# Optimization experiments

Measured on AMD Instinct MI355X. Metric: run time of the kernel, lower is better.

## Reference

```python
import jax, jax.numpy as jnp
import numpy as np

H = 128; TIME_DIM = 8; LAM = 0.01; NUM_LAYERS = 2; B = 64
N_FACT = 100000; N_COMP = 5000; E = 500000; D_FACT = 384; D_COMP = 64
MLP_IN = 2 + 2 * (TIME_DIM // 2) + 1  # 11


def setup_inputs() -> dict:
    key = jax.random.key(0)
    ks = jax.random.split(key, 40)
    rn = lambda k, sh, s=0.05: jax.random.normal(k, sh, jnp.float32) * s
    inp = {
        'x_fact': jax.random.normal(ks[0], (N_FACT, D_FACT), jnp.float32),
        'x_comp': jax.random.normal(ks[1], (N_COMP, D_COMP), jnp.float32),
        'ea_f2c': jax.random.uniform(ks[2], (E, 2), jnp.float32),
        'ea_c2f': jax.random.uniform(ks[3], (E, 2), jnp.float32),
        'ei_f2c_src': jax.random.randint(ks[4], (E,), 0, N_FACT, jnp.int32),
        'ei_f2c_dst': jax.random.randint(ks[5], (E,), 0, N_COMP, jnp.int32),
        'ei_c2f_src': jax.random.randint(ks[6], (E,), 0, N_COMP, jnp.int32),
        'ei_c2f_dst': jax.random.randint(ks[7], (E,), 0, N_FACT, jnp.int32),
        'fact_batch': jnp.sort(jax.random.randint(ks[8], (N_FACT,), 0, B, jnp.int32)),
        'comp_batch': jnp.sort(jax.random.randint(ks[9], (N_COMP,), 0, B, jnp.int32)),
        # lazy per-type input projections
        'W_in_fact': rn(ks[10], (D_FACT, H)), 'b_in_fact': jnp.zeros((H,), jnp.float32),
        'W_in_comp': rn(ks[11], (D_COMP, H)), 'b_in_comp': jnp.zeros((H,), jnp.float32),
        # EdgeAttrEncoder MLP: 11 -> 32 -> 16 -> 1
        'eW1': rn(ks[12], (MLP_IN, 32)), 'eb1': jnp.zeros((32,), jnp.float32),
        'eW2': rn(ks[13], (32, 16)), 'eb2': jnp.zeros((16,), jnp.float32),
        'eW3': rn(ks[14], (16, 1)), 'eb3': jnp.zeros((1,), jnp.float32),
        # GraphConv per layer (axis0) per edge type (axis1: 0=f->c, 1=c->f)
        'W_rel': rn(ks[15], (NUM_LAYERS, 2, H, H)), 'b_rel': jnp.zeros((NUM_LAYERS, 2, H), jnp.float32),
        'W_root': rn(ks[16], (NUM_LAYERS, 2, H, H)),
        # shared post LayerNorm per node type (axis0: 0=fact, 1=company)
        'ln_scale': jnp.ones((2, H), jnp.float32), 'ln_bias': jnp.zeros((2, H), jnp.float32),
        # classifier 2H -> H -> 1
        'Wc1': rn(ks[17], (2 * H, H)), 'bc1': jnp.zeros((H,), jnp.float32),
        'Wc2': rn(ks[18], (H, 1)), 'bc2': jnp.zeros((1,), jnp.float32),
    }
    return inp


def _edge_gate(ea, eW1, eb1, eW2, eb2, eW3, eb3):
    # ea: [E,2] -> gate [E]
    sent = jnp.clip(ea[:, 0:1], -1.0, 1.0)
    decay = ea[:, 1:2]
    # decay in [0,1] -> delta_t = -log(decay)/lambda, clamped >= 0
    dt = jnp.maximum(-jnp.log(jnp.clip(decay, 1e-6, None)) / LAM, 0.0)
    ds = jnp.clip(dt / 30.0, 0.0, 12.0)
    freqs = jnp.arange(1, TIME_DIM // 2 + 1, dtype=ds.dtype)
    tvec = jnp.concatenate([jnp.sin(ds * freqs), jnp.cos(ds * freqs), ds], axis=-1)
    x = jnp.concatenate([sent, jnp.log1p(dt), tvec], axis=-1)  # [E,11]
    h = jax.nn.relu(x @ eW1 + eb1)
    h = jax.nn.relu(h @ eW2 + eb2)
    return jax.nn.sigmoid(h @ eW3 + eb3)[:, 0]


def _layernorm(x, scale, bias, eps=1e-5):
    mu = jnp.mean(x, axis=-1, keepdims=True)
    var = jnp.var(x, axis=-1, keepdims=True)
    return (x - mu) * jax.lax.rsqrt(var + eps) * scale + bias


def _seg_mean(x, seg, n):
    s = jax.ops.segment_sum(x, seg, num_segments=n)
    c = jax.ops.segment_sum(jnp.ones((x.shape[0], 1), x.dtype), seg, num_segments=n)
    return s / jnp.maximum(c, 1.0)


def reference(x_fact, x_comp, ea_f2c, ea_c2f, ei_f2c_src, ei_f2c_dst, ei_c2f_src,
              ei_c2f_dst, fact_batch, comp_batch, W_in_fact, b_in_fact, W_in_comp,
              b_in_comp, eW1, eb1, eW2, eb2, eW3, eb3, W_rel, b_rel, W_root,
              ln_scale, ln_bias, Wc1, bc1, Wc2, bc2):
    # per-type input projection + ReLU
    xf = jax.nn.relu(x_fact @ W_in_fact + b_in_fact)   # [N_fact, H]
    xc = jax.nn.relu(x_comp @ W_in_comp + b_in_comp)   # [N_comp, H]
    # MLP-gated edge weights (shared encoder across relations)
    w_f2c = _edge_gate(ea_f2c, eW1, eb1, eW2, eb2, eW3, eb3)  # [E]
    w_c2f = _edge_gate(ea_c2f, eW1, eb1, eW2, eb2, eW3, eb3)  # [E]
    nf, nc = xf.shape[0], xc.shape[0]
    for l in range(NUM_LAYERS):
        prev_f, prev_c = xf, xc
        # GraphConv: lin_rel(sum_j w_ij * x_j) + lin_root(x_i)  (aggr='add')
        agg_c = jax.ops.segment_sum(xf[ei_f2c_src] * w_f2c[:, None], ei_f2c_dst, num_segments=nc)
        new_c = agg_c @ W_rel[l, 0] + b_rel[l, 0] + xc @ W_root[l, 0]
        agg_f = jax.ops.segment_sum(xc[ei_c2f_src] * w_c2f[:, None], ei_c2f_dst, num_segments=nf)
        new_f = agg_f @ W_rel[l, 1] + b_rel[l, 1] + xf @ W_root[l, 1]
        # ReLU -> residual -> shared per-type LayerNorm
        xf = _layernorm(jax.nn.relu(new_f) + prev_f, ln_scale[0], ln_bias[0])
        xc = _layernorm(jax.nn.relu(new_c) + prev_c, ln_scale[1], ln_bias[1])
    fact_pool = _seg_mean(xf, fact_batch, B)   # [B, H]
    comp_pool = _seg_mean(xc, comp_batch, B)   # [B, H]
    pooled = jnp.concatenate([fact_pool, comp_pool], axis=-1)  # [B, 2H]
    h = jax.nn.relu(pooled @ Wc1 + bc1)
    return (h @ Wc2 + bc2)[:, 0]  # [B] logits
```

## Files before the change

kernel.cpp:

```cpp
#include <hip/hip_runtime.h>
#include <math.h>

#define H 128
#define EDGES 500000
#define NFACT 100000
#define NCOMP 5000
#define BATCH 64
#define NTILE 6250

typedef _Float16 half8_t __attribute__((ext_vector_type(8)));
typedef float floatx4 __attribute__((ext_vector_type(4)));

__device__ inline short4 f4_to_h4(float4 v){
  union { short4 s; _Float16 h[4]; } u;
  u.h[0]=(_Float16)v.x; u.h[1]=(_Float16)v.y; u.h[2]=(_Float16)v.z; u.h[3]=(_Float16)v.w;
  return u.s;
}

__global__ __launch_bounds__(1024) void k_scan1(const int* __restrict__ cnt, int n,
                                                int* __restrict__ offs, int* __restrict__ part){
  __shared__ int sh[1024];
  int tid = threadIdx.x;
  int i = blockIdx.x*1024 + tid;
  int v = (i < n) ? cnt[i] : 0;
  sh[tid] = v;
  __syncthreads();
  for (int d = 1; d < 1024; d <<= 1){
    int t = (tid >= d) ? sh[tid-d] : 0;
    __syncthreads();
    sh[tid] += t;
    __syncthreads();
  }
  if (i < n) offs[i] = sh[tid] - v;
  if (tid == 1023) part[blockIdx.x] = sh[1023];
}

__global__ void k_scan2(int* part, int nb){
  __shared__ int sh[128];
  int tid = threadIdx.x;
  int v = (tid < nb) ? part[tid] : 0;
  sh[tid] = v;
  __syncthreads();
  for (int d = 1; d < 128; d <<= 1){
    int t = (tid >= d) ? sh[tid-d] : 0;
    __syncthreads();
    sh[tid] += t;
    __syncthreads();
  }
  if (tid < nb) part[tid] = sh[tid] - v;
}

__global__ __launch_bounds__(1024) void k_scan3(int* offs, int n, const int* __restrict__ part, int total){
  int i = blockIdx.x*1024 + threadIdx.x;
  if (i < n) offs[i] += part[blockIdx.x];
  if (i == 0) offs[n] = total;
}

__global__ void k_fill2d(const int* __restrict__ src0, const int* __restrict__ dst0,
                         const float* __restrict__ w0, const int* __restrict__ offs0,
                         int* __restrict__ cur0, int4* __restrict__ ed0,
                         const int* __restrict__ src1, const int* __restrict__ dst1,
                         const float* __restrict__ w1, const int* __restrict__ offs1,
                         int* __restrict__ cur1, int4* __restrict__ ed1, int n){
  int half = gridDim.x >> 1;
  int dir = blockIdx.x >= half;
  const int* src = dir ? src1 : src0;
  const int* dst = dir ? dst1 : dst0;
  const float* w = dir ? w1 : w0;
  const int* offs = dir ? offs1 : offs0;
  int* cur = dir ? cur1 : cur0;
  int4* ed = dir ? ed1 : ed0;
  int bid = blockIdx.x - (dir ? half : 0);
  for (int e = bid*blockDim.x + threadIdx.x; e < n; e += half*blockDim.x){
    int d = dst[e];
    int p = offs[d] + atomicAdd(&cur[d], 1);
    ed[p] = make_int4(src[e], __float_as_int(w[e]), d, 0);
  }
}

__global__ __launch_bounds__(256) void k_prep(const float* __restrict__ W_in,
                                              const float* __restrict__ W_rel,
                                              const float* __restrict__ W_root,
                                              _Float16* __restrict__ wt_in,
                                              _Float16* __restrict__ wcat0,
                                              _Float16* __restrict__ wcat1){
  int i = blockIdx.x*256 + threadIdx.x;
  if (i < 49152){
    int n = i / 384, k = i % 384;
    wt_in[i] = (_Float16)W_in[k*128 + n];
  } else if (i < 49152 + 32768){
    int j = i - 49152;
    int n = j / 256, k = j % 256;
    const float* Wr = W_rel  + 1*16384;
    const float* Wo = W_root + 1*16384;
    wcat0[j] = (_Float16)(k < 128 ? Wr[k*128+n] : Wo[(k-128)*128+n]);
  } else if (i < 49152 + 65536){
    int j = i - 49152 - 32768;
    int n = j / 256, k = j % 256;
    const float* Wr = W_rel  + 3*16384;
    const float* Wo = W_root + 3*16384;
    wcat1[j] = (_Float16)(k < 128 ? Wr[k*128+n] : Wo[(k-128)*128+n]);
  }
}

__global__ __launch_bounds__(256) void k_gate2(const float* __restrict__ ea0,
                       const float* __restrict__ ea1,
                       const int* __restrict__ dst0, const int* __restrict__ dst1,
                       int* __restrict__ cnt0, int* __restrict__ cnt1,
                       const float* __restrict__ eW1, const float* __restrict__ eb1,
                       const float* __restrict__ eW2, const float* __restrict__ eb2,
                       const float* __restrict__ eW3, const float* __restrict__ eb3,
                       float* __restrict__ wout0, float* __restrict__ wout1, int n){
  __shared__ float w1t[32*12];
  __shared__ float w2s[32*16];
  __shared__ float b1s[32], b2s[16], w3s[16];
  __shared__ float b3s;
  int tid = threadIdx.x;
  for (int i = tid; i < 352; i += 256){
    int k = i >> 5, c = i & 31;
    w1t[c*12 + k] = eW1[i];
  }
  if (tid < 32) w1t[tid*12 + 11] = 0.f;
  for (int i = tid; i < 512; i += 256) w2s[i] = eW2[i];
  if (tid < 32) b1s[tid] = eb1[tid];
  if (tid < 16) b2s[tid] = eb2[tid];
  if (tid < 16) w3s[tid] = eW3[tid];
  if (tid == 0) b3s = eb3[0];
  __syncthreads();

  int half = gridDim.x >> 1;
  int dir = blockIdx.x >= half;
  const float* ea = dir ? ea1 : ea0;
  const int* dst  = dir ? dst1 : dst0;
  int* cnt        = dir ? cnt1 : cnt0;
  float* wout     = dir ? wout1 : wout0;
  int bid = blockIdx.x - (dir ? half : 0);

  const float4* w1t4 = (const float4*)w1t;
  const float4* w24  = (const float4*)w2s;
  float4 b2v0 = ((const float4*)b2s)[0], b2v1 = ((const float4*)b2s)[1];
  float4 b2v2 = ((const float4*)b2s)[2], b2v3 = ((const float4*)b2s)[3];
  float4 w3v0 = ((const float4*)w3s)[0], w3v1 = ((const float4*)w3s)[1];
  float4 w3v2 = ((const float4*)w3s)[2], w3v3 = ((const float4*)w3s)[3];

  for (int e = bid*blockDim.x + tid; e < n; e += half*blockDim.x){
    float2 eav = ((const float2*)ea)[e];
    float sent  = fminf(fmaxf(eav.x, -1.f), 1.f);
    float decay = eav.y;
    float dt = fmaxf(-__logf(fmaxf(decay, 1e-6f)) * 100.f, 0.f);
    float ds = fminf(dt * (1.f/30.f), 12.f);
    float s1 = __sinf(ds), c1 = __cosf(ds);
    float s2v = 2.f*s1*c1;
    float c2v = 1.f - 2.f*s1*s1;
    float s3v = s1*c2v + c1*s2v;
    float c3v = c1*c2v - s1*s2v;
    float s4v = 2.f*s2v*c2v;
    float c4v = 1.f - 2.f*s2v*s2v;
    float4 x0 = make_float4(sent, __logf(1.f + dt), s1, s2v);
    float4 x1 = make_float4(s3v, s4v, c1, c2v);
    float4 x2 = make_float4(c3v, c4v, ds, 0.f);

    float4 sa = b2v0, sb = b2v1, sc = b2v2, sd = b2v3;
    #pragma unroll 2
    for (int i = 0; i < 32; i++){
      float4 wa = w1t4[i*3+0], wb = w1t4[i*3+1], wc = w1t4[i*3+2];
      float h = b1s[i];
      h += x0.x*wa.x + x0.y*wa.y + x0.z*wa.z + x0.w*wa.w;
      h += x1.x*wb.x + x1.y*wb.y + x1.z*wb.z + x1.w*wb.w;
      h += x2.x*wc.x + x2.y*wc.y + x2.z*wc.z;
      h = fmaxf(h, 0.f);
      float4 va = w24[i*4+0], vb = w24[i*4+1], vc = w24[i*4+2], vd = w24[i*4+3];
      sa.x += h*va.x; sa.y += h*va.y; sa.z += h*va.z; sa.w += h*va.w;
      sb.x += h*vb.x; sb.y += h*vb.y; sb.z += h*vb.z; sb.w += h*vb.w;
      sc.x += h*vc.x; sc.y += h*vc.y; sc.z += h*vc.z; sc.w += h*vc.w;
      sd.x += h*vd.x; sd.y += h*vd.y; sd.z += h*vd.z; sd.w += h*vd.w;
    }
    float o = b3s;
    o += fmaxf(sa.x,0.f)*w3v0.x + fmaxf(sa.y,0.f)*w3v0.y + fmaxf(sa.z,0.f)*w3v0.z + fmaxf(sa.w,0.f)*w3v0.w;
    o += fmaxf(sb.x,0.f)*w3v1.x + fmaxf(sb.y,0.f)*w3v1.y + fmaxf(sb.z,0.f)*w3v1.z + fmaxf(sb.w,0.f)*w3v1.w;
    o += fmaxf(sc.x,0.f)*w3v2.x + fmaxf(sc.y,0.f)*w3v2.y + fmaxf(sc.z,0.f)*w3v2.z + fmaxf(sc.w,0.f)*w3v2.w;
    o += fmaxf(sd.x,0.f)*w3v3.x + fmaxf(sd.y,0.f)*w3v3.y + fmaxf(sd.z,0.f)*w3v3.z + fmaxf(sd.w,0.f)*w3v3.w;
    wout[e] = __fdividef(1.f, 1.f + __expf(-o));
    atomicAdd(&cnt[dst[e]], 1);
  }
}

template<int K, int R>
__global__ __launch_bounds__(128) void k_input_s(const float* __restrict__ X, const float* __restrict__ W,
                                                 const float* __restrict__ bias, float* __restrict__ Y){
  __shared__ float xs[R*K];
  int t = threadIdx.x;
  long row0 = (long)blockIdx.x * R;
  const float4* src = (const float4*)(X + row0*K);
  float4* d4 = (float4*)xs;
  for (int i = t; i < R*K/4; i += 128) d4[i] = src[i];
  __syncthreads();
  float acc[R];
  #pragma unroll
  for (int r = 0; r < R; r++) acc[r] = 0.f;
  for (int k4 = 0; k4 < K/4; k4++){
    int kb = k4*4;
    float w0 = W[(kb+0)*H+t], w1 = W[(kb+1)*H+t], w2 = W[(kb+2)*H+t], w3 = W[(kb+3)*H+t];
    #pragma unroll
    for (int r = 0; r < R; r++){
      float4 xv = ((const float4*)(xs + r*K))[k4];
      acc[r] += xv.x*w0 + xv.y*w1 + xv.z*w2 + xv.w*w3;
    }
  }
  float b = bias[t];
  #pragma unroll
  for (int r = 0; r < R; r++)
    Y[(row0+r)*H + t] = fmaxf(acc[r] + b, 0.f);
}

__global__ __launch_bounds__(256, 2) void k_input_m(const float* __restrict__ X,
                                                 const _Float16* __restrict__ Wt,
                                                 const float* __restrict__ bias,
                                                 float* __restrict__ Y){
  __shared__ _Float16 xs[16][392];
  __shared__ float tb[4*16*36];
  int t = threadIdx.x;
  int lane = t & 63, wv = t >> 6;
  int m = lane & 15, q = lane >> 4;

  half8_t wreg[2][12];
  float bcol[2];
  #pragma unroll
  for (int j = 0; j < 2; j++){
    int col = (wv*2 + j)*16 + m;
    const _Float16* wb = Wt + (size_t)col*384 + q*8;
    #pragma unroll
    for (int ks = 0; ks < 12; ks++) wreg[j][ks] = *(const half8_t*)(wb + ks*32);
    bcol[j] = bias[col];
  }

  int row_i[6], c4_i[6];
  #pragma unroll
  for (int i = 0; i < 6; i++){
    int idx = i*256 + t;
    row_i[i] = idx/96; c4_i[i] = idx - row_i[i]*96;
  }

  int tpb = (NTILE + gridDim.x - 1)/gridDim.x;
  int tb0 = blockIdx.x*tpb, tb1 = tb0 + tpb;
  if (tb1 > NTILE) tb1 = NTILE;
  if (tb0 >= tb1) return;

  const float4* X4 = (const float4*)X;
  float4 r[6];
  #pragma unroll
  for (int i = 0; i < 6; i++) r[i] = X4[(size_t)tb0*1536 + i*256 + t];

  float* tbw = &tb[wv*576];
  int rowl = lane >> 2, c8l = lane & 3;

  for (int tile = tb0; tile < tb1; ++tile){
    __syncthreads();
    #pragma unroll
    for (int i = 0; i < 6; i++)
      *(short4*)&xs[row_i[i]][c4_i[i]*4] = f4_to_h4(r[i]);
    __syncthreads();
    if (tile + 1 < tb1){
      size_t base = (size_t)(tile+1)*1536;
      #pragma unroll
      for (int i = 0; i < 6; i++) r[i] = X4[base + i*256 + t];
    }
    __builtin_amdgcn_sched_barrier(0);

    floatx4 acc0 = (floatx4){0.f,0.f,0.f,0.f};
    floatx4 acc1 = (floatx4){0.f,0.f,0.f,0.f};
    #pragma unroll
    for (int ks = 0; ks < 12; ks++){
      half8_t av = *(const half8_t*)&xs[m][ks*32 + q*8];
      acc0 = __builtin_amdgcn_mfma_f32_16x16x32_f16(av, wreg[0][ks], acc0, 0, 0, 0);
      acc1 = __builtin_amdgcn_mfma_f32_16x16x32_f16(av, wreg[1][ks], acc1, 0, 0, 0);
    }
    long rb = (long)tile*16;
    #pragma unroll
    for (int j = 0; j < 2; j++){
      floatx4 a = j ? acc1 : acc0;
      int lc = j*16 + m;
      #pragma unroll
      for (int i2 = 0; i2 < 4; i2++)
        tbw[(q*4+i2)*36 + lc] = fmaxf(a[i2] + bcol[j], 0.f);
    }
    __syncthreads();
    {
      const float* srcp = tbw + rowl*36 + c8l*8;
      float* dstp = Y + (rb + rowl)*H + wv*32 + c8l*8;
      *(float4*)dstp       = *(const float4*)(srcp);
      *(float4*)(dstp + 4) = *(const float4*)(srcp + 4);
    }
  }
}

__global__ __launch_bounds__(64) void k_layer_m(
    const float* __restrict__ xsrc, const float* __restrict__ xprev,
    const int* __restrict__ offs, const int4* __restrict__ ed,
    const _Float16* __restrict__ Wt, const float* __restrict__ brel,
    const float* __restrict__ lnsc, const float* __restrict__ lnbi,
    float* __restrict__ xnext){
  __shared__ _Float16 xin[16][264];
  __shared__ float tb[16*144];
  int t = threadIdx.x, c = t & 31, g = t >> 5;
  long row0 = (long)blockIdx.x * 16;
  int grow0 = g*8;
  #pragma unroll
  for (int j = 0; j < 8; j++){
    int lr = grow0 + j;
    ((short4*)&xin[lr][0])[c] = make_short4(0,0,0,0);
    float4 pv = ((const float4*)(xprev + (row0+lr)*H))[c];
    ((short4*)&xin[lr][128])[c] = f4_to_h4(pv);
  }
  int lo = offs[row0 + grow0], hi = offs[row0 + grow0 + 8];
  float4 a = make_float4(0.f,0.f,0.f,0.f);
  int cur = (int)row0 + grow0;
  int idx = lo;
  for (; idx + 8 <= hi; idx += 8){
    int4 mrec[8];
    #pragma unroll
    for (int j = 0; j < 8; j++) mrec[j] = ed[idx+j];
    float4 v[8];
    #pragma unroll
    for (int j = 0; j < 8; j++) v[j] = ((const float4*)(xsrc + (long)mrec[j].x*H))[c];
    #pragma unroll
    for (int j = 0; j < 8; j++){
      float w = __int_as_float(mrec[j].y);
      if (mrec[j].z != cur){ ((short4*)&xin[cur-(int)row0][0])[c] = f4_to_h4(a); a = make_float4(0.f,0.f,0.f,0.f); cur = mrec[j].z; }
      a.x += v[j].x*w; a.y += v[j].y*w; a.z += v[j].z*w; a.w += v[j].w*w;
    }
  }
  for (; idx < hi; idx++){
    int4 mrec = ed[idx];
    float4 v = ((const float4*)(xsrc + (long)mrec.x*H))[c];
    float w = __int_as_float(mrec.y);
    if (mrec.z != cur){ ((short4*)&xin[cur-(int)row0][0])[c] = f4_to_h4(a); a = make_float4(0.f,0.f,0.f,0.f); cur = mrec.z; }
    a.x += v.x*w; a.y += v.y*w; a.z += v.z*w; a.w += v.w*w;
  }
  if (lo < hi) ((short4*)&xin[cur-(int)row0][0])[c] = f4_to_h4(a);

  int m = t & 15, q = t >> 4;
  floatx4 acc[8];
  #pragma unroll
  for (int nt = 0; nt < 8; nt++) acc[nt] = (floatx4){0.f,0.f,0.f,0.f};
  #pragma unroll
  for (int ks = 0; ks < 8; ks++){
    half8_t av = *(const half8_t*)&xin[m][ks*32 + q*8];
    #pragma unroll
    for (int nt = 0; nt < 8; nt++){
      half8_t bv = *(const half8_t*)(Wt + (size_t)(nt*16 + m)*256 + ks*32 + q*8);
      acc[nt] = __builtin_amdgcn_mfma_f32_16x16x32_f16(av, bv, acc[nt], 0, 0, 0);
    }
  }
  float vs[8][4];
  float s[4] = {0.f,0.f,0.f,0.f}, ss[4] = {0.f,0.f,0.f,0.f};
  #pragma unroll
  for (int nt = 0; nt < 8; nt++){
    int col = nt*16 + m;
    float b = brel[col];
    #pragma unroll
    for (int i = 0; i < 4; i++){
      int lr = q*4 + i;
      float pv = (float)xin[lr][128 + col];
      float v = fmaxf(acc[nt][i] + b, 0.f) + pv;
      vs[nt][i] = v;
      s[i] += v; ss[i] += v*v;
    }
  }
  #pragma unroll
  for (int i = 0; i < 4; i++){
    #pragma unroll
    for (int mm = 1; mm < 16; mm <<= 1){
      s[i]  += __shfl_xor(s[i],  mm, 64);
      ss[i] += __shfl_xor(ss[i], mm, 64);
    }
  }
  #pragma unroll
  for (int nt = 0; nt < 8; nt++){
    int col = nt*16 + m;
    float lsc = lnsc[col], lbi = lnbi[col];
    int chnk = col >> 5, lc = col & 31;
    #pragma unroll
    for (int i = 0; i < 4; i++){
      float mu  = s[i]*(1.f/H);
      float var = ss[i]*(1.f/H) - mu*mu;
      float rstd = rsqrtf(var + 1e-5f);
      tb[(q*4+i)*144 + chnk*36 + lc] = (vs[nt][i] - mu)*rstd*lsc + lbi;
    }
  }
  __syncthreads();
  {
    int rowl = t >> 2, c8 = t & 3;
    const float* srcp = &tb[rowl*144 + c8*36];
    float4* dst4 = (float4*)(xnext + (row0 + rowl)*H + c8*32);
    #pragma unroll
    for (int k = 0; k < 8; k++)
      dst4[k] = *(const float4*)(srcp + k*4);
  }
}

template<int R>
__global__ __launch_bounds__(128) void k_layer(
    const float* __restrict__ xsrc, const float* __restrict__ xprev,
    const int* __restrict__ offs, const int4* __restrict__ ed,
    const float* __restrict__ Wrel, const float* __restrict__ brel,
    const float* __restrict__ Wroot, const float* __restrict__ lnsc,
    const float* __restrict__ lnbi, float* __restrict__ xnext){
  constexpr int RG = R/4;
  __shared__ float xin[R][256];
  int t = threadIdx.x, c = t & 31, g = t >> 5;
  long row0 = (long)blockIdx.x * R;
  int grow0 = g*RG;
  #pragma unroll
  for (int j = 0; j < RG; j++){
    int lr = grow0 + j;
    ((float4*)&xin[lr][0])[c] = make_float4(0.f,0.f,0.f,0.f);
    ((float4*)&xin[lr][128])[c] = ((const float4*)(xprev + (row0+lr)*H))[c];
  }
  int lo = offs[row0 + grow0], hi = offs[row0 + grow0 + RG];
  float4 a = make_float4(0.f,0.f,0.f,0.f);
  int cur = (int)row0 + grow0;
  int idx = lo;
  for (; idx + 8 <= hi; idx += 8){
    int4 m[8];
    #pragma unroll
    for (int j = 0; j < 8; j++) m[j] = ed[idx+j];
    float4 v[8];
    #pragma unroll
    for (int j = 0; j < 8; j++) v[j] = ((const float4*)(xsrc + (long)m[j].x*H))[c];
    #pragma unroll
    for (int j = 0; j < 8; j++){
      float w = __int_as_float(m[j].y);
      if (m[j].z != cur){ ((float4*)&xin[cur-(int)row0][0])[c] = a; a = make_float4(0.f,0.f,0.f,0.f); cur = m[j].z; }
      a.x += v[j].x*w; a.y += v[j].y*w; a.z += v[j].z*w; a.w += v[j].w*w;
    }
  }
  for (; idx < hi; idx++){
    int4 m = ed[idx];
    float4 v = ((const float4*)(xsrc + (long)m.x*H))[c];
    float w = __int_as_float(m.y);
    if (m.z != cur){ ((float4*)&xin[cur-(int)row0][0])[c] = a; a = make_float4(0.f,0.f,0.f,0.f); cur = m.z; }
    a.x += v.x*w; a.y += v.y*w; a.z += v.z*w; a.w += v.w*w;
  }
  if (lo < hi) ((float4*)&xin[cur-(int)row0][0])[c] = a;

  float4 acc[RG];
  float4 bv = ((const float4*)brel)[c];
  #pragma unroll
  for (int j = 0; j < RG; j++) acc[j] = bv;
  #pragma unroll
  for (int p = 0; p < 2; p++){
    const float4* Wp = (const float4*)(p ? Wroot : Wrel) + c;
    #pragma unroll 4
    for (int k4 = 0; k4 < 32; k4++){
      float4 xv[RG];
      #pragma unroll
      for (int j = 0; j < RG; j++)
        xv[j] = ((const float4*)xin[grow0+j])[p*32 + k4];
      #pragma unroll
      for (int kk = 0; kk < 4; kk++){
        float4 wv = Wp[(size_t)(k4*4+kk)*32];
        #pragma unroll
        for (int j = 0; j < RG; j++){
          float xk = (kk==0) ? xv[j].x : (kk==1) ? xv[j].y : (kk==2) ? xv[j].z : xv[j].w;
          acc[j].x += xk*wv.x; acc[j].y += xk*wv.y; acc[j].z += xk*wv.z; acc[j].w += xk*wv.w;
        }
      }
    }
  }
  float4 lsc = ((const float4*)lnsc)[c];
  float4 lbi = ((const float4*)lnbi)[c];
  #pragma unroll
  for (int j = 0; j < RG; j++){
    int lr = grow0 + j;
    float4 pv = ((const float4*)&xin[lr][128])[c];
    float4 v;
    v.x = fmaxf(acc[j].x, 0.f) + pv.x;
    v.y = fmaxf(acc[j].y, 0.f) + pv.y;
    v.z = fmaxf(acc[j].z, 0.f) + pv.z;
    v.w = fmaxf(acc[j].w, 0.f) + pv.w;
    float s  = v.x + v.y + v.z + v.w;
    float ss = v.x*v.x + v.y*v.y + v.z*v.z + v.w*v.w;
    #pragma unroll
    for (int mm = 1; mm < 32; mm <<= 1){ s += __shfl_xor(s, mm, 64); ss += __shfl_xor(ss, mm, 64); }
    float mu  = s*(1.f/H);
    float var = ss*(1.f/H) - mu*mu;
    float rstd = rsqrtf(var + 1e-5f);
    float4 o;
    o.x = (v.x - mu)*rstd*lsc.x + lbi.x;
    o.y = (v.y - mu)*rstd*lsc.y + lbi.y;
    o.z = (v.z - mu)*rstd*lsc.z + lbi.z;
    o.w = (v.w - mu)*rstd*lsc.w + lbi.w;
    ((float4*)(xnext + (row0+lr)*H))[c] = o;
  }
}

#define PCHUNK 128
#define FBLK ((NFACT + PCHUNK - 1) / PCHUNK)
#define CBLK ((NCOMP + PCHUNK - 1) / PCHUNK)

__global__ __launch_bounds__(128) void k_pool_acc(const float* __restrict__ xf, const float* __restrict__ xc,
                                                  const int* __restrict__ fb, const int* __restrict__ cb,
                                                  float* __restrict__ pooled){
  int t = threadIdx.x;
  int b = blockIdx.x;
  if (b < FBLK){
    int start = b*PCHUNK, end = start + PCHUNK; if (end > NFACT) end = NFACT;
    float s = 0.f; int curb = -1;
    for (int i = start; i < end; i++){
      int bb = fb[i];
      if (bb != curb){
        if (curb >= 0) atomicAdd(&pooled[curb*256 + t], s);
        curb = bb; s = 0.f;
      }
      s += xf[(long)i*H + t];
    }
    if (curb >= 0) atomicAdd(&pooled[curb*256 + t], s);
  } else {
    int bbk = b - FBLK;
    int start = bbk*PCHUNK, end = start + PCHUNK; if (end > NCOMP) end = NCOMP;
    float s = 0.f; int curb = -1;
    for (int i = start; i < end; i++){
      int bb = cb[i];
      if (bb != curb){
        if (curb >= 0) atomicAdd(&pooled[curb*256 + 128 + t], s);
        curb = bb; s = 0.f;
      }
      s += xc[(long)i*H + t];
    }
    if (curb >= 0) atomicAdd(&pooled[curb*256 + 128 + t], s);
  }
}

__device__ inline int lowerb(const int* a, int n, int key){
  int lo = 0, hi = n;
  while (lo < hi){ int m = (lo+hi) >> 1; if (a[m] < key) lo = m+1; else hi = m; }
  return lo;
}

__global__ __launch_bounds__(128) void k_head(const float* __restrict__ pooled,
                                              const int* __restrict__ fb, const int* __restrict__ cb,
                                              const float* __restrict__ Wc1, const float* __restrict__ bc1,
                                              const float* __restrict__ Wc2, const float* __restrict__ bc2,
                                              float* __restrict__ out){
  __shared__ float p[256];
  __shared__ float red[2];
  int t = threadIdx.x, b = blockIdx.x;
  int flo = lowerb(fb, NFACT, b), fhi = lowerb(fb, NFACT, b+1);
  int clo = lowerb(cb, NCOMP, b), chi = lowerb(cb, NCOMP, b+1);
  float fc = (float)((fhi - flo) > 1 ? (fhi - flo) : 1);
  float cc = (float)((chi - clo) > 1 ? (chi - clo) : 1);
  p[t]       = pooled[b*256 + t] / fc;
  p[128 + t] = pooled[b*256 + 128 + t] / cc;
  __syncthreads();
  float acc = bc1[t];
  #pragma unroll 4
  for (int k = 0; k < 256; k++) acc += p[k]*Wc1[k*H + t];
  float h = fmaxf(acc, 0.f)*Wc2[t];
  #pragma unroll
  for (int m = 1; m < 64; m <<= 1) h += __shfl_xor(h, m, 64);
  if ((t & 63) == 0) red[t>>6] = h;
  __syncthreads();
  if (t == 0) out[b] = red[0] + red[1] + bc2[0];
}

extern "C" void kernel_launch(void* const* d_in, const int* in_sizes, int n_in,
                              void* d_out, int out_size, void* d_ws, size_t ws_size,
                              hipStream_t stream){
  const float* x_fact = (const float*)d_in[0];
  const float* x_comp = (const float*)d_in[1];
  const float* ea_f2c = (const float*)d_in[2];
  const float* ea_c2f = (const float*)d_in[3];
  const int* s_f2c   = (const int*)d_in[4];
  const int* dst_f2c = (const int*)d_in[5];
  const int* s_c2f   = (const int*)d_in[6];
  const int* dst_c2f = (const int*)d_in[7];
  const int* fb = (const int*)d_in[8];
  const int* cb = (const int*)d_in[9];
  const float* W_in_f = (const float*)d_in[10];
  const float* b_in_f = (const float*)d_in[11];
  const float* W_in_c = (const float*)d_in[12];
  const float* b_in_c = (const float*)d_in[13];
  const float* eW1 = (const float*)d_in[14]; const float* eb1 = (const float*)d_in[15];
  const float* eW2 = (const float*)d_in[16]; const float* eb2 = (const float*)d_in[17];
  const float* eW3 = (const float*)d_in[18]; const float* eb3 = (const float*)d_in[19];
  const float* W_rel = (const float*)d_in[20]; const float* b_rel = (const float*)d_in[21];
  const float* W_root = (const float*)d_in[22];
  const float* ln_s = (const float*)d_in[23]; const float* ln_b = (const float*)d_in[24];
  const float* Wc1 = (const float*)d_in[25]; const float* bc1 = (const float*)d_in[26];
  const float* Wc2 = (const float*)d_in[27]; const float* bc2 = (const float*)d_in[28];
  float* out = (float*)d_out;

  char* ws = (char*)d_ws;
  size_t off = 0;
  auto alloc = [&](size_t bytes)->char*{ char* p = ws + off; off = (off + bytes + 255) & ~(size_t)255; return p; };
  float* xf0   = (float*)alloc((size_t)NFACT*H*4);
  float* xf1   = (float*)alloc((size_t)NFACT*H*4);
  float* xc0   = (float*)alloc((size_t)NCOMP*H*4);
  float* xc1   = (float*)alloc((size_t)NCOMP*H*4);
  float* w_f2c = (float*)alloc((size_t)EDGES*4);
  float* w_c2f = (float*)alloc((size_t)EDGES*4);
  int4* ed_f2c = (int4*)alloc((size_t)EDGES*16);
  int4* ed_c2f = (int4*)alloc((size_t)EDGES*16);
  int* off_f2c = (int*)alloc((size_t)(NCOMP+1)*4);
  int* cur_f2c = (int*)alloc((size_t)NCOMP*4);
  int* off_c2f = (int*)alloc((size_t)(NFACT+1)*4);
  int* cur_c2f = (int*)alloc((size_t)NFACT*4);
  int* part    = (int*)alloc(128*4);
  float* pooled= (float*)alloc((size_t)BATCH*256*4);
  _Float16* wt_in = (_Float16*)alloc((size_t)49152*2);
  _Float16* wcat0 = (_Float16*)alloc((size_t)32768*2);
  _Float16* wcat1 = (_Float16*)alloc((size_t)32768*2);

  k_prep<<<448,256,0,stream>>>(W_in_f, W_rel, W_root, wt_in, wcat0, wcat1);
  hipMemsetAsync(cur_f2c, 0, NCOMP*4, stream);
  hipMemsetAsync(cur_c2f, 0, NFACT*4, stream);
  k_gate2<<<1024,256,0,stream>>>(ea_f2c, ea_c2f, dst_f2c, dst_c2f,
                                 cur_f2c, cur_c2f,
                                 eW1,eb1,eW2,eb2,eW3,eb3, w_f2c, w_c2f, EDGES);

  {
    int nb = (NCOMP + 1023)/1024;
    k_scan1<<<nb,1024,0,stream>>>(cur_f2c, NCOMP, off_f2c, part);
    k_scan2<<<1,128,0,stream>>>(part, nb);
    k_scan3<<<nb,1024,0,stream>>>(off_f2c, NCOMP, part, EDGES);
  }
  {
    int nb = (NFACT + 1023)/1024;
    k_scan1<<<nb,1024,0,stream>>>(cur_c2f, NFACT, off_c2f, part);
    k_scan2<<<1,128,0,stream>>>(part, nb);
    k_scan3<<<nb,1024,0,stream>>>(off_c2f, NFACT, part, EDGES);
  }
  hipMemsetAsync(cur_f2c, 0, NCOMP*4, stream);
  hipMemsetAsync(cur_c2f, 0, NFACT*4, stream);
  k_fill2d<<<1024,256,0,stream>>>(s_f2c, dst_f2c, w_f2c, off_f2c, cur_f2c, ed_f2c,
                                  s_c2f, dst_c2f, w_c2f, off_c2f, cur_c2f, ed_c2f, EDGES);

  k_input_m<<<512,256,0,stream>>>(x_fact, wt_in, b_in_f, xf0);
  k_input_s<64,8><<<NCOMP/8,128,0,stream>>>(x_comp, W_in_c, b_in_c, xc0);

  const float* xf_p = xf0; const float* xc_p = xc0;
  float* xf_n = xf1; float* xc_n = xc1;
  for (int l = 0; l < 2; l++){
    const float* Wr0 = W_rel  + (size_t)(l*2+0)*H*H;
    const float* br0 = b_rel  + (size_t)(l*2+0)*H;
    const float* br1 = b_rel  + (size_t)(l*2+1)*H;
    const float* Wo0 = W_root + (size_t)(l*2+0)*H*H;
    const _Float16* wcat = (l == 0) ? wcat0 : wcat1;
    k_layer<4><<<NCOMP/4,128,0,stream>>>(xf_p, xc_p, off_f2c, ed_f2c,
                                         Wr0, br0, Wo0, ln_s + H, ln_b + H, xc_n);
    k_layer_m<<<NFACT/16,64,0,stream>>>(xc_p, xf_p, off_c2f, ed_c2f,
                                        wcat, br1, ln_s, ln_b, xf_n);
    const float* tf = xf_p; xf_p = xf_n; xf_n = (float*)tf;
    const float* tc = xc_p; xc_p = xc_n; xc_n = (float*)tc;
  }

  hipMemsetAsync(pooled, 0, (size_t)BATCH*256*4, stream);
  k_pool_acc<<<FBLK + CBLK,128,0,stream>>>(xf_p, xc_p, fb, cb, pooled);
  k_head<<<BATCH,128,0,stream>>>(pooled, fb, cb, Wc1, bc1, Wc2, bc2, out);
}
```

Measured before the change: 798.4 us.

## Pack four independent wave tiles per block and prefetch edge records in c2f layer

The fact-side layer kernel now launches 256-thread blocks in which each 64-lane wave handles its own 16-row tile. Each wave's fp16 input buffer aliases its LayerNorm staging buffer, so shared memory per wave shrinks and the block-wide barrier is replaced by compiler memory fences. The edge loop also double-buffers the next eight edge records so index loads overlap the gathers. The risks are that dropping the barrier relies on wave-synchronous LDS behaviour within one wave, and the extra prefetch registers could lower occupancy.

```diff
diff --git a/kernel.cpp b/kernel.cpp
--- a/kernel.cpp
+++ b/kernel.cpp
@@ -294,16 +294,21 @@
   }
 }
 
-__global__ __launch_bounds__(64) void k_layer_m(
+__global__ __launch_bounds__(256) void k_layer_m(
     const float* __restrict__ xsrc, const float* __restrict__ xprev,
     const int* __restrict__ offs, const int4* __restrict__ ed,
     const _Float16* __restrict__ Wt, const float* __restrict__ brel,
     const float* __restrict__ lnsc, const float* __restrict__ lnbi,
     float* __restrict__ xnext){
-  __shared__ _Float16 xin[16][264];
-  __shared__ float tb[16*144];
-  int t = threadIdx.x, c = t & 31, g = t >> 5;
-  long row0 = (long)blockIdx.x * 16;
+  __shared__ float tball[4*2304];
+  int t = threadIdx.x;
+  int lane = t & 63, wv = t >> 6;
+  long tile = (long)blockIdx.x*4 + wv;
+  if (tile*16 >= NFACT) return;
+  long row0 = tile*16;
+  float* tb = tball + wv*2304;
+  _Float16 (*xin)[264] = reinterpret_cast<_Float16 (*)[264]>(tb);
+  int c = lane & 31, g = lane >> 5;
   int grow0 = g*8;
   #pragma unroll
   for (int j = 0; j < 8; j++){
@@ -316,19 +321,31 @@
   float4 a = make_float4(0.f,0.f,0.f,0.f);
   int cur = (int)row0 + grow0;
   int idx = lo;
-  for (; idx + 8 <= hi; idx += 8){
-    int4 mrec[8];
-    #pragma unroll
-    for (int j = 0; j < 8; j++) mrec[j] = ed[idx+j];
+  int nb = (hi - lo) >> 3;
+  int4 rec[8];
+  if (nb > 0){
+    #pragma unroll
+    for (int j = 0; j < 8; j++) rec[j] = ed[idx+j];
+  }
+  for (int b = 0; b < nb; b++){
+    int nxt = idx + 8;
+    int4 rec2[8];
+    if (b + 1 < nb){
+      #pragma unroll
+      for (int j = 0; j < 8; j++) rec2[j] = ed[nxt+j];
+    }
     float4 v[8];
     #pragma unroll
-    for (int j = 0; j < 8; j++) v[j] = ((const float4*)(xsrc + (long)mrec[j].x*H))[c];
+    for (int j = 0; j < 8; j++) v[j] = ((const float4*)(xsrc + (long)rec[j].x*H))[c];
     #pragma unroll
     for (int j = 0; j < 8; j++){
-      float w = __int_as_float(mrec[j].y);
-      if (mrec[j].z != cur){ ((short4*)&xin[cur-(int)row0][0])[c] = f4_to_h4(a); a = make_float4(0.f,0.f,0.f,0.f); cur = mrec[j].z; }
+      float w = __int_as_float(rec[j].y);
+      if (rec[j].z != cur){ ((short4*)&xin[cur-(int)row0][0])[c] = f4_to_h4(a); a = make_float4(0.f,0.f,0.f,0.f); cur = rec[j].z; }
       a.x += v[j].x*w; a.y += v[j].y*w; a.z += v[j].z*w; a.w += v[j].w*w;
     }
+    #pragma unroll
+    for (int j = 0; j < 8; j++) rec[j] = rec2[j];
+    idx = nxt;
   }
   for (; idx < hi; idx++){
     int4 mrec = ed[idx];
@@ -339,7 +356,7 @@
   }
   if (lo < hi) ((short4*)&xin[cur-(int)row0][0])[c] = f4_to_h4(a);
 
-  int m = t & 15, q = t >> 4;
+  int m = lane & 15, q = lane >> 4;
   floatx4 acc[8];
   #pragma unroll
   for (int nt = 0; nt < 8; nt++) acc[nt] = (floatx4){0.f,0.f,0.f,0.f};
@@ -375,6 +392,7 @@
       ss[i] += __shfl_xor(ss[i], mm, 64);
     }
   }
+  asm volatile("" ::: "memory");
   #pragma unroll
   for (int nt = 0; nt < 8; nt++){
     int col = nt*16 + m;
@@ -388,9 +406,9 @@
       tb[(q*4+i)*144 + chnk*36 + lc] = (vs[nt][i] - mu)*rstd*lsc + lbi;
     }
   }
-  __syncthreads();
+  asm volatile("" ::: "memory");
   {
-    int rowl = t >> 2, c8 = t & 3;
+    int rowl = lane >> 2, c8 = lane & 3;
     const float* srcp = &tb[rowl*144 + c8*36];
     float4* dst4 = (float4*)(xnext + (row0 + rowl)*H + c8*32);
     #pragma unroll
@@ -649,8 +667,8 @@
     const _Float16* wcat = (l == 0) ? wcat0 : wcat1;
     k_layer<4><<<NCOMP/4,128,0,stream>>>(xf_p, xc_p, off_f2c, ed_f2c,
                                          Wr0, br0, Wo0, ln_s + H, ln_b + H, xc_n);
-    k_layer_m<<<NFACT/16,64,0,stream>>>(xc_p, xf_p, off_c2f, ed_c2f,
-                                        wcat, br1, ln_s, ln_b, xf_n);
+    k_layer_m<<<(NTILE+3)/4,256,0,stream>>>(xc_p, xf_p, off_c2f, ed_c2f,
+                                            wcat, br1, ln_s, ln_b, xf_n);
     const float* tf = xf_p; xf_p = xf_n; xf_n = (float*)tf;
     const float* tc = xc_p; xc_p = xc_n; xc_n = (float*)tc;
   }
```

New measurement: 803.6 us. No clear change (+0.6%).
